# Performance work log

Measured on AMD Instinct MI355X. Metric: run time of the kernel, lower is better.

Reference implementation:

```python
import jax, jax.numpy as jnp
import numpy as np

CL = 64      # per-object feature dim
N = 8        # num objects/slots
B = 8192     # batch


def _init(key, fan_in, shape):
    # torch Linear default: U(-1/sqrt(fan_in), 1/sqrt(fan_in))
    bound = 1.0 / np.sqrt(fan_in)
    return jax.random.uniform(key, shape, jnp.float32, -bound, bound)


def setup_inputs() -> dict:
    key = jax.random.key(0)
    ks = jax.random.split(key, 20)
    inp = {
        "s": jax.random.normal(ks[0], (B, N, CL), jnp.float32),
        # weights stored (in, out); y = x @ W + b
        "W_enc": _init(ks[1], CL, (CL, CL)),   "b_enc": _init(ks[2], CL, (CL,)),
        "W_self0": _init(ks[3], CL, (CL, CL)), "b_self0": _init(ks[4], CL, (CL,)),
        "W_self1": _init(ks[5], CL, (CL, CL)), "b_self1": _init(ks[6], CL, (CL,)),
        "W_rel0": _init(ks[7], 2 * CL + 1, (2 * CL + 1, 2 * CL)), "b_rel0": _init(ks[8], 2 * CL + 1, (2 * CL,)),
        "W_rel1": _init(ks[9], 2 * CL, (2 * CL, CL)),             "b_rel1": _init(ks[10], 2 * CL, (CL,)),
        "W_rel2": _init(ks[11], CL, (CL, CL)),                    "b_rel2": _init(ks[12], CL, (CL,)),
        "W_att0": _init(ks[13], 2 * CL + 1, (2 * CL + 1, 2 * CL)), "b_att0": _init(ks[14], 2 * CL + 1, (2 * CL,)),
        "W_att1": _init(ks[15], 2 * CL, (2 * CL, CL)),             "b_att1": _init(ks[16], 2 * CL, (CL,)),
        "W_att2": _init(ks[17], CL, (CL, 1)),                      "b_att2": _init(ks[18], CL, (1,)),
    }
    return inp


def reference(s, W_enc, b_enc, W_self0, b_self0, W_self1, b_self1,
              W_rel0, b_rel0, W_rel1, b_rel1, W_rel2, b_rel2,
              W_att0, b_att0, W_att1, b_att1, W_att2, b_att2):
    elu = jax.nn.elu
    # keep first 2 coords (positions), re-encode the rest
    s = jnp.concatenate([s[..., :2], (s @ W_enc + b_enc)[..., 2:]], axis=-1)  # [B,N,CL]

    # self dynamics
    h = elu(s @ W_self0 + b_self0)
    self_dyn = h @ W_self1 + b_self1 + h                                      # [B,N,CL]

    # pairwise squared distances on first two coords: [B,N,N,1]
    pos = s[..., :2]
    dist = jnp.sum((pos[:, :, None, :] - pos[:, None, :, :]) ** 2, axis=-1, keepdims=True)

    # combinations = cat(arg1_i, arg2_j, dist). Split the first linear's weight rows
    # so we never materialize the [B,N,N,2CL+1] concat tensor.
    def pair_linear(W, b):
        Wa, Wb, Wd = W[:CL], W[CL:2 * CL], W[2 * CL]
        return (s @ Wa)[:, :, None, :] + (s @ Wb)[:, None, :, :] + dist * Wd + b

    rel_h1 = elu(pair_linear(W_rel0, b_rel0))        # [B,N,N,2CL]
    rel_h2 = elu(rel_h1 @ W_rel1 + b_rel1)           # [B,N,N,CL]
    rel_f = rel_h2 @ W_rel2 + b_rel2 + rel_h2        # [B,N,N,CL]

    att = elu(pair_linear(W_att0, b_att0))
    att = elu(att @ W_att1 + b_att1)
    att = jax.nn.sigmoid(att @ W_att2 + b_att2)      # [B,N,N,1]

    diag_mask = (1.0 - jnp.eye(N, dtype=s.dtype))[None, :, :, None]
    rel_dyn = jnp.sum(rel_f * diag_mask * att, axis=2)   # [B,N,CL]

    return jnp.sum(self_dyn + rel_dyn, axis=1)           # [B,CL]
```

## Files before the change

### kernel.cpp

```cpp
#include <hip/hip_runtime.h>
#include <math.h>

constexpr int NCL = 64;
constexpr int NN  = 8;
constexpr int NG  = 4;
constexpr int NT  = 1024;

typedef __attribute__((ext_vector_type(4))) float f32x4;
typedef __attribute__((ext_vector_type(8))) short s16x8;
#define MFMA __builtin_amdgcn_mfma_f32_16x16x32_bf16

constexpr int OFF_ENC = 0;
constexpr int OFF_S0  = 1024;
constexpr int OFF_S1  = 2048;
constexpr int OFF_R0  = 3072;
constexpr int OFF_A0  = 7168;
constexpr int OFF_A1  = 11264;
constexpr int OFF_R1  = 13312;

__device__ __forceinline__ float elu_f(float x) { return x > 0.f ? x : __expf(x) - 1.f; }

__device__ __forceinline__ short bfh_rn(float x) {
    union { float f; unsigned u; } c; c.f = x;
    return (short)((c.u + 0x7fffu + ((c.u >> 16) & 1u)) >> 16);
}
__device__ __forceinline__ void split_tr(float x, short& hi, short& lo) {
    union { float f; unsigned u; } c; c.f = x;
    hi = (short)(c.u >> 16);
    union { unsigned u; float f; } t; t.u = c.u & 0xffff0000u;
    lo = bfh_rn(x - t.f);
}

__device__ __forceinline__ void afrag_split(const float* act, int row, int kbase,
                                            s16x8& hi, s16x8& lo) {
    const float4 v0 = *(const float4*)(act + row * 68 + kbase);
    const float4 v1 = *(const float4*)(act + row * 68 + kbase + 4);
    float v[8] = {v0.x, v0.y, v0.z, v0.w, v1.x, v1.y, v1.z, v1.w};
    #pragma unroll
    for (int e = 0; e < 8; ++e) { short a, b; split_tr(v[e], a, b); hi[e] = a; lo[e] = b; }
}

__device__ __forceinline__ f32x4 node_tile_pk(const float* act, const s16x8* __restrict__ wb,
                                              int mt, int nt, int lane) {
    const int row = mt * 16 + (lane & 15);
    const int g   = lane >> 4;
    f32x4 acc = {0.f, 0.f, 0.f, 0.f};
    #pragma unroll
    for (int kg = 0; kg < 2; ++kg) {
        s16x8 ah, al;
        afrag_split(act, row, kg * 32 + g * 8, ah, al);
        const s16x8 bh = wb[(kg * 4 + nt) * 64 + lane];
        const s16x8 bl = wb[512 + (kg * 4 + nt) * 64 + lane];
        acc = MFMA(ah, bh, acc, 0, 0, 0);
        acc = MFMA(ah, bl, acc, 0, 0, 0);
        acc = MFMA(al, bh, acc, 0, 0, 0);
    }
    return acc;
}

__device__ __forceinline__ void x1frag(const float* Arow, const float* Brow,
                                       const float* wdg, float d, int fbase,
                                       s16x8& hi, s16x8& lo) {
    const float4 a0 = *(const float4*)(Arow + fbase);
    const float4 a1 = *(const float4*)(Arow + fbase + 4);
    const float4 c0 = *(const float4*)(Brow + fbase);
    const float4 c1 = *(const float4*)(Brow + fbase + 4);
    const float4 w0 = *(const float4*)(wdg + fbase);
    const float4 w1 = *(const float4*)(wdg + fbase + 4);
    float v[8];
    v[0] = elu_f(a0.x + c0.x + d * w0.x);
    v[1] = elu_f(a0.y + c0.y + d * w0.y);
    v[2] = elu_f(a0.z + c0.z + d * w0.z);
    v[3] = elu_f(a0.w + c0.w + d * w0.w);
    v[4] = elu_f(a1.x + c1.x + d * w1.x);
    v[5] = elu_f(a1.y + c1.y + d * w1.y);
    v[6] = elu_f(a1.z + c1.z + d * w1.z);
    v[7] = elu_f(a1.w + c1.w + d * w1.w);
    #pragma unroll
    for (int e = 0; e < 8; ++e) { short a, b; split_tr(v[e], a, b); hi[e] = a; lo[e] = b; }
}

__global__ __launch_bounds__(64)
void prep_kernel(const float* __restrict__ We,  const float* __restrict__ Ws0,
                 const float* __restrict__ Ws1, const float* __restrict__ Wr0,
                 const float* __restrict__ Wa0, const float* __restrict__ Wa1,
                 const float* __restrict__ Wr1, s16x8* __restrict__ ws)
{
    const int b = blockIdx.x, lane = threadIdx.x;
    const float* W; int nnt, nfrag, base, frag;
    if      (b < 8)   { W = We;  nnt = 4; nfrag = 8;  base = OFF_ENC; frag = b; }
    else if (b < 16)  { W = Ws0; nnt = 4; nfrag = 8;  base = OFF_S0;  frag = b - 8; }
    else if (b < 24)  { W = Ws1; nnt = 4; nfrag = 8;  base = OFF_S1;  frag = b - 16; }
    else if (b < 56)  { W = Wr0; nnt = 8; nfrag = 32; base = OFF_R0;  frag = b - 24; }
    else if (b < 88)  { W = Wa0; nnt = 8; nfrag = 32; base = OFF_A0;  frag = b - 56; }
    else if (b < 104) { W = Wa1; nnt = 4; nfrag = 16; base = OFF_A1;  frag = b - 88; }
    else              { W = Wr1; nnt = 4; nfrag = 16; base = OFF_R1;  frag = b - 104; }
    const int kg = frag / nnt, nt = frag % nnt;
    const int N  = nnt * 16;
    const int g  = lane >> 4, col = nt * 16 + (lane & 15);
    s16x8 hi, lo;
    #pragma unroll
    for (int e = 0; e < 8; ++e) {
        short a, c; split_tr(W[(kg * 32 + g * 8 + e) * N + col], a, c);
        hi[e] = a; lo[e] = c;
    }
    ws[base + frag * 64 + lane]              = hi;
    ws[base + nfrag * 64 + frag * 64 + lane] = lo;
}

__global__ __launch_bounds__(NT, 1)
void gh_kernel(const float* __restrict__ S,
               const float* __restrict__ b_enc,
               const float* __restrict__ b_self0, const float* __restrict__ b_self1,
               const float* __restrict__ W_rel0,  const float* __restrict__ b_rel0,
               const float* __restrict__ b_rel1,
               const float* __restrict__ W_rel2,  const float* __restrict__ b_rel2,
               const float* __restrict__ W_att0,  const float* __restrict__ b_att0,
               const float* __restrict__ b_att1,
               const float* __restrict__ W_att2,  const float* __restrict__ b_att2,
               const s16x8* __restrict__ wp,
               float* __restrict__ Out)
{
    __shared__ __align__(16) float sbuf[32 * 68];
    __shared__ __align__(16) float encb[32 * 68];
    __shared__ __align__(16) float hbuf[32 * 68];
    __shared__ __align__(16) float ABm[4][32 * 132];
    __shared__ __align__(16) s16x8 wstp[2048];
    __shared__ float d2l[4 * 64];
    __shared__ float cntl[32];
    __shared__ float Ubuf[4 * 68];
    __shared__ float wdl[2][128];

    const int tid  = threadIdx.x;
    const int w    = tid >> 6;
    const int lane = tid & 63;
    const int g    = lane >> 4;
    const int b0   = blockIdx.x * NG;
    float* sd = sbuf;
    float* Tb = hbuf;

    {
        const float* src = S + (size_t)b0 * NN * NCL;
        for (int idx = tid; idx < 32 * 64; idx += NT)
            sbuf[(idx >> 6) * 68 + (idx & 63)] = src[idx];
        for (int idx = tid; idx < 2048; idx += NT)
            wstp[idx] = wp[OFF_A1 + idx];
        if (tid < 128) {
            wdl[0][tid] = W_rel0[128 * 128 + tid];
            wdl[1][tid] = W_att0[128 * 128 + tid];
        }
    }
    __syncthreads();

    if (tid < 256) {
        const int bi = tid >> 6, i = (tid >> 3) & 7, j = tid & 7;
        const float dx = sbuf[(bi * 8 + i) * 68 + 0] - sbuf[(bi * 8 + j) * 68 + 0];
        const float dy = sbuf[(bi * 8 + i) * 68 + 1] - sbuf[(bi * 8 + j) * 68 + 1];
        d2l[bi * 64 + i * 8 + j] = dx * dx + dy * dy;
    }

    if (w < 8) {
        const int mt = w & 1, nt = w >> 1;
        f32x4 acc = node_tile_pk(sbuf, wp + OFF_ENC, mt, nt, lane);
        const int   col = nt * 16 + (lane & 15);
        const float be  = b_enc[col];
        #pragma unroll
        for (int reg = 0; reg < 4; ++reg) {
            const int row = mt * 16 + g * 4 + reg;
            float v = acc[reg] + be;
            if (col < 2) v = sbuf[row * 68 + col];
            encb[row * 68 + col] = v;
        }
    }
    __syncthreads();

    if (w < 8) {
        const int mt = w & 1, nt = w >> 1;
        f32x4 acc = node_tile_pk(encb, wp + OFF_S0, mt, nt, lane);
        const int   col = nt * 16 + (lane & 15);
        const float bs  = b_self0[col];
        #pragma unroll
        for (int reg = 0; reg < 4; ++reg)
            hbuf[(mt * 16 + g * 4 + reg) * 68 + col] = elu_f(acc[reg] + bs);
    }
    __syncthreads();

    if (w < 8) {
        const int mt = w & 1, nt = w >> 1;
        f32x4 acc = node_tile_pk(hbuf, wp + OFF_S1, mt, nt, lane);
        const int   col = nt * 16 + (lane & 15);
        const float bs  = b_self1[col];
        #pragma unroll
        for (int reg = 0; reg < 4; ++reg) {
            const int row = mt * 16 + g * 4 + reg;
            sd[row * 68 + col] = acc[reg] + bs + hbuf[row * 68 + col];
        }
    }
    {
        const int mtp = w >> 3, ntp = w & 7;
        const int row = mtp * 16 + (lane & 15);
        const int col = ntp * 16 + (lane & 15);
        s16x8 eh[2], el[2];
        afrag_split(encb, row, g * 8, eh[0], el[0]);
        afrag_split(encb, row, 32 + g * 8, eh[1], el[1]);
        #pragma unroll
        for (int m = 0; m < 4; ++m) {
            const s16x8* wb = wp + ((m < 2) ? OFF_R0 : OFF_A0);
            const int kgo = (m & 1) * 2;
            f32x4 acc = {0.f, 0.f, 0.f, 0.f};
            #pragma unroll
            for (int kg = 0; kg < 2; ++kg) {
                const s16x8 bh = wb[((kgo + kg) * 8 + ntp) * 64 + lane];
                const s16x8 bl = wb[2048 + ((kgo + kg) * 8 + ntp) * 64 + lane];
                acc = MFMA(eh[kg], bh, acc, 0, 0, 0);
                acc = MFMA(eh[kg], bl, acc, 0, 0, 0);
                acc = MFMA(el[kg], bh, acc, 0, 0, 0);
            }
            const float badd = (m == 0) ? b_rel0[col] : (m == 2) ? b_att0[col] : 0.f;
            #pragma unroll
            for (int reg = 0; reg < 4; ++reg)
                ABm[m][(mtp * 16 + g * 4 + reg) * 132 + col] = acc[reg] + badd;
        }
    }
    __syncthreads();

    const int bi    = w >> 2;
    const int ihalf = (w >> 1) & 1;
    const int mt    = w & 1;
    const int pp    = (lane & 15) + 16 * mt;
    const int il    = pp >> 3, jj8 = pp & 7;
    const float* Arow_a = &ABm[2][(bi * 8 + ihalf * 4 + il) * 132];
    const float* Brow_a = &ABm[3][(bi * 8 + jj8) * 132];
    const float* Arow_r = &ABm[0][(bi * 8 + ihalf * 4 + il) * 132];
    const float* Brow_r = &ABm[1][(bi * 8 + jj8) * 132];
    const float dpair   = d2l[bi * 64 + (ihalf * 4 + il) * 8 + jj8];

    float attreg[4];
    {
        const float ba2 = b_att2[0];
        float wa2v[4], ba1v[4];
        #pragma unroll
        for (int nt = 0; nt < 4; ++nt) {
            wa2v[nt] = W_att2[nt * 16 + (lane & 15)];
            ba1v[nt] = b_att1[nt * 16 + (lane & 15)];
        }
        s16x8 ah[4], al[4];
        #pragma unroll
        for (int kg = 0; kg < 4; ++kg)
            x1frag(Arow_a, Brow_a, &wdl[1][0], dpair, kg * 32 + g * 8, ah[kg], al[kg]);
        f32x4 acc[4];
        #pragma unroll
        for (int nt = 0; nt < 4; ++nt) {
            acc[nt] = {ba1v[nt], ba1v[nt], ba1v[nt], ba1v[nt]};
            #pragma unroll
            for (int kg = 0; kg < 4; ++kg) {
                const s16x8 bh = wstp[(kg * 4 + nt) * 64 + lane];
                const s16x8 bl = wstp[1024 + (kg * 4 + nt) * 64 + lane];
                acc[nt] = MFMA(ah[kg], bh, acc[nt], 0, 0, 0);
                acc[nt] = MFMA(ah[kg], bl, acc[nt], 0, 0, 0);
                acc[nt] = MFMA(al[kg], bh, acc[nt], 0, 0, 0);
            }
        }
        #pragma unroll
        for (int reg = 0; reg < 4; ++reg) {
            float s = 0.f;
            #pragma unroll
            for (int nt = 0; nt < 4; ++nt) s += elu_f(acc[nt][reg]) * wa2v[nt];
            s += __shfl_xor(s, 1, 64);
            s += __shfl_xor(s, 2, 64);
            s += __shfl_xor(s, 4, 64);
            s += __shfl_xor(s, 8, 64);
            attreg[reg] = 1.f / (1.f + __expf(-(s + ba2)));
        }
    }
    __syncthreads();

    for (int idx = tid; idx < 2048; idx += NT)
        wstp[idx] = wp[OFF_R1 + idx];
    __syncthreads();

    {
        float br1v[4];
        #pragma unroll
        for (int nt = 0; nt < 4; ++nt) br1v[nt] = b_rel1[nt * 16 + (lane & 15)];
        s16x8 ah[4], al[4];
        #pragma unroll
        for (int kg = 0; kg < 4; ++kg)
            x1frag(Arow_r, Brow_r, &wdl[0][0], dpair, kg * 32 + g * 8, ah[kg], al[kg]);
        f32x4 acc[4];
        #pragma unroll
        for (int nt = 0; nt < 4; ++nt) {
            acc[nt] = {br1v[nt], br1v[nt], br1v[nt], br1v[nt]};
            #pragma unroll
            for (int kg = 0; kg < 4; ++kg) {
                const s16x8 bh = wstp[(kg * 4 + nt) * 64 + lane];
                const s16x8 bl = wstp[1024 + (kg * 4 + nt) * 64 + lane];
                acc[nt] = MFMA(ah[kg], bh, acc[nt], 0, 0, 0);
                acc[nt] = MFMA(ah[kg], bl, acc[nt], 0, 0, 0);
                acc[nt] = MFMA(al[kg], bh, acc[nt], 0, 0, 0);
            }
        }
        const int ifull = ihalf * 4 + 2 * mt + (g >> 1);
        float coef[4], cpart = 0.f;
        #pragma unroll
        for (int reg = 0; reg < 4; ++reg) {
            const int jj = 4 * (g & 1) + reg;
            coef[reg] = (jj == ifull) ? 0.f : attreg[reg];
            cpart += coef[reg];
        }
        const float csum = cpart + __shfl_xor(cpart, 16, 64);
        if (((g & 1) == 0) && ((lane & 15) == 0))
            cntl[bi * 8 + ifull] = csum;
        #pragma unroll
        for (int nt = 0; nt < 4; ++nt) {
            float tpart = 0.f;
            #pragma unroll
            for (int reg = 0; reg < 4; ++reg)
                tpart += coef[reg] * elu_f(acc[nt][reg]);
            const float tsum = tpart + __shfl_xor(tpart, 16, 64);
            if ((g & 1) == 0)
                Tb[(bi * 8 + ifull) * 68 + nt * 16 + (lane & 15)] = tsum;
        }
    }
    __syncthreads();

    if (tid < 256) {
        const int b = tid >> 6, c = tid & 63;
        float u = 0.f;
        #pragma unroll
        for (int i = 0; i < 8; ++i) u += Tb[(b * 8 + i) * 68 + c];
        Ubuf[b * 68 + c] = u;
    }
    __syncthreads();

    if (tid < 256) {
        const int b = tid >> 6, c = tid & 63;
        float sds = 0.f, C = 0.f;
        #pragma unroll
        for (int i = 0; i < 8; ++i) {
            sds += sd[(b * 8 + i) * 68 + c];
            C   += cntl[b * 8 + i];
        }
        float r = 0.f;
        #pragma unroll 8
        for (int k = 0; k < 64; ++k)
            r += Ubuf[b * 68 + k] * W_rel2[k * 64 + c];
        Out[(size_t)(b0 + b) * 64 + c] = sds + r + C * b_rel2[c] + Ubuf[b * 68 + c];
    }
}

extern "C" void kernel_launch(void* const* d_in, const int* in_sizes, int n_in,
                              void* d_out, int out_size, void* d_ws, size_t ws_size,
                              hipStream_t stream) {
    const float* S       = (const float*)d_in[0];
    const float* W_enc   = (const float*)d_in[1];
    const float* b_enc   = (const float*)d_in[2];
    const float* W_self0 = (const float*)d_in[3];
    const float* b_self0 = (const float*)d_in[4];
    const float* W_self1 = (const float*)d_in[5];
    const float* b_self1 = (const float*)d_in[6];
    const float* W_rel0  = (const float*)d_in[7];
    const float* b_rel0  = (const float*)d_in[8];
    const float* W_rel1  = (const float*)d_in[9];
    const float* b_rel1  = (const float*)d_in[10];
    const float* W_rel2  = (const float*)d_in[11];
    const float* b_rel2  = (const float*)d_in[12];
    const float* W_att0  = (const float*)d_in[13];
    const float* b_att0  = (const float*)d_in[14];
    const float* W_att1  = (const float*)d_in[15];
    const float* b_att1  = (const float*)d_in[16];
    const float* W_att2  = (const float*)d_in[17];
    const float* b_att2  = (const float*)d_in[18];

    s16x8* wpk = (s16x8*)d_ws;

    prep_kernel<<<dim3(120), dim3(64), 0, stream>>>(
        W_enc, W_self0, W_self1, W_rel0, W_att0, W_att1, W_rel1, wpk);

    const int nB   = in_sizes[0] / (NN * NCL);
    const int grid = nB / NG;

    gh_kernel<<<dim3(grid), dim3(NT), 0, stream>>>(
        S, b_enc, b_self0, b_self1,
        W_rel0, b_rel0, b_rel1, W_rel2, b_rel2,
        W_att0, b_att0, b_att1, W_att2, b_att2,
        wpk, (float*)d_out);
}
```

Baseline: 245.0 us.

## Double-buffer pair weights in LDS, stream fragments, and use MFMA for rel2 projection

Keeps the att1 and rel1 packed weights in two separate LDS buffers so the mid-kernel reload and its two barriers go away. Builds the bf16 hi/lo activation fragments one k-group at a time using a perm-based pack, which lowers register pressure. The final W_rel2 projection moves from a scalar 64-term loop over global memory to split-bf16 MFMAs on weights packed by the prep kernel. This costs extra LDS and an additional barrier, and the lo-part rounding changes from round-to-nearest to truncation, with slight precision differences.

```diff
diff --git a/kernel.cpp b/kernel.cpp
--- a/kernel.cpp
+++ b/kernel.cpp
@@ -17,27 +17,31 @@
 constexpr int OFF_A0  = 7168;
 constexpr int OFF_A1  = 11264;
 constexpr int OFF_R1  = 13312;
+constexpr int OFF_R2  = 15360;
 
 __device__ __forceinline__ float elu_f(float x) { return x > 0.f ? x : __expf(x) - 1.f; }
 
-__device__ __forceinline__ short bfh_rn(float x) {
-    union { float f; unsigned u; } c; c.f = x;
-    return (short)((c.u + 0x7fffu + ((c.u >> 16) & 1u)) >> 16);
-}
-__device__ __forceinline__ void split_tr(float x, short& hi, short& lo) {
-    union { float f; unsigned u; } c; c.f = x;
-    hi = (short)(c.u >> 16);
-    union { unsigned u; float f; } t; t.u = c.u & 0xffff0000u;
-    lo = bfh_rn(x - t.f);
+__device__ __forceinline__ unsigned f2u(float x) { union { float f; unsigned u; } c; c.f = x; return c.u; }
+__device__ __forceinline__ float u2f(unsigned u) { union { unsigned u; float f; } c; c.u = u; return c.f; }
+
+__device__ __forceinline__ void splitpack8(const float v[8], s16x8& hi, s16x8& lo) {
+    union { s16x8 s; unsigned u[4]; } H, L;
+    #pragma unroll
+    for (int e = 0; e < 8; e += 2) {
+        H.u[e >> 1] = __builtin_amdgcn_perm(f2u(v[e + 1]), f2u(v[e]), 0x07060302u);
+        const float t0 = u2f(f2u(v[e])     & 0xffff0000u);
+        const float t1 = u2f(f2u(v[e + 1]) & 0xffff0000u);
+        L.u[e >> 1] = __builtin_amdgcn_perm(f2u(v[e + 1] - t1), f2u(v[e] - t0), 0x07060302u);
+    }
+    hi = H.s; lo = L.s;
 }
 
 __device__ __forceinline__ void afrag_split(const float* act, int row, int kbase,
                                             s16x8& hi, s16x8& lo) {
     const float4 v0 = *(const float4*)(act + row * 68 + kbase);
     const float4 v1 = *(const float4*)(act + row * 68 + kbase + 4);
-    float v[8] = {v0.x, v0.y, v0.z, v0.w, v1.x, v1.y, v1.z, v1.w};
-    #pragma unroll
-    for (int e = 0; e < 8; ++e) { short a, b; split_tr(v[e], a, b); hi[e] = a; lo[e] = b; }
+    const float v[8] = {v0.x, v0.y, v0.z, v0.w, v1.x, v1.y, v1.z, v1.w};
+    splitpack8(v, hi, lo);
 }
 
 __device__ __forceinline__ f32x4 node_tile_pk(const float* act, const s16x8* __restrict__ wb,
@@ -68,23 +72,34 @@
     const float4 w0 = *(const float4*)(wdg + fbase);
     const float4 w1 = *(const float4*)(wdg + fbase + 4);
     float v[8];
-    v[0] = elu_f(a0.x + c0.x + d * w0.x);
-    v[1] = elu_f(a0.y + c0.y + d * w0.y);
-    v[2] = elu_f(a0.z + c0.z + d * w0.z);
-    v[3] = elu_f(a0.w + c0.w + d * w0.w);
-    v[4] = elu_f(a1.x + c1.x + d * w1.x);
-    v[5] = elu_f(a1.y + c1.y + d * w1.y);
-    v[6] = elu_f(a1.z + c1.z + d * w1.z);
-    v[7] = elu_f(a1.w + c1.w + d * w1.w);
-    #pragma unroll
-    for (int e = 0; e < 8; ++e) { short a, b; split_tr(v[e], a, b); hi[e] = a; lo[e] = b; }
+    v[0] = elu_f(fmaf(d, w0.x, a0.x + c0.x));
+    v[1] = elu_f(fmaf(d, w0.y, a0.y + c0.y));
+    v[2] = elu_f(fmaf(d, w0.z, a0.z + c0.z));
+    v[3] = elu_f(fmaf(d, w0.w, a0.w + c0.w));
+    v[4] = elu_f(fmaf(d, w1.x, a1.x + c1.x));
+    v[5] = elu_f(fmaf(d, w1.y, a1.y + c1.y));
+    v[6] = elu_f(fmaf(d, w1.z, a1.z + c1.z));
+    v[7] = elu_f(fmaf(d, w1.w, a1.w + c1.w));
+    splitpack8(v, hi, lo);
+}
+
+__device__ __forceinline__ short bfh_rn(float x) {
+    union { float f; unsigned u; } c; c.f = x;
+    return (short)((c.u + 0x7fffu + ((c.u >> 16) & 1u)) >> 16);
+}
+__device__ __forceinline__ void split_tr(float x, short& hi, short& lo) {
+    union { float f; unsigned u; } c; c.f = x;
+    hi = (short)(c.u >> 16);
+    union { unsigned u; float f; } t; t.u = c.u & 0xffff0000u;
+    lo = bfh_rn(x - t.f);
 }
 
 __global__ __launch_bounds__(64)
 void prep_kernel(const float* __restrict__ We,  const float* __restrict__ Ws0,
                  const float* __restrict__ Ws1, const float* __restrict__ Wr0,
                  const float* __restrict__ Wa0, const float* __restrict__ Wa1,
-                 const float* __restrict__ Wr1, s16x8* __restrict__ ws)
+                 const float* __restrict__ Wr1, const float* __restrict__ Wr2,
+                 s16x8* __restrict__ ws)
 {
     const int b = blockIdx.x, lane = threadIdx.x;
     const float* W; int nnt, nfrag, base, frag;
@@ -94,7 +109,8 @@
     else if (b < 56)  { W = Wr0; nnt = 8; nfrag = 32; base = OFF_R0;  frag = b - 24; }
     else if (b < 88)  { W = Wa0; nnt = 8; nfrag = 32; base = OFF_A0;  frag = b - 56; }
     else if (b < 104) { W = Wa1; nnt = 4; nfrag = 16; base = OFF_A1;  frag = b - 88; }
-    else              { W = Wr1; nnt = 4; nfrag = 16; base = OFF_R1;  frag = b - 104; }
+    else if (b < 120) { W = Wr1; nnt = 4; nfrag = 16; base = OFF_R1;  frag = b - 104; }
+    else              { W = Wr2; nnt = 4; nfrag = 8;  base = OFF_R2;  frag = b - 120; }
     const int kg = frag / nnt, nt = frag % nnt;
     const int N  = nnt * 16;
     const int g  = lane >> 4, col = nt * 16 + (lane & 15);
@@ -113,8 +129,7 @@
                const float* __restrict__ b_enc,
                const float* __restrict__ b_self0, const float* __restrict__ b_self1,
                const float* __restrict__ W_rel0,  const float* __restrict__ b_rel0,
-               const float* __restrict__ b_rel1,
-               const float* __restrict__ W_rel2,  const float* __restrict__ b_rel2,
+               const float* __restrict__ b_rel1,  const float* __restrict__ b_rel2,
                const float* __restrict__ W_att0,  const float* __restrict__ b_att0,
                const float* __restrict__ b_att1,
                const float* __restrict__ W_att2,  const float* __restrict__ b_att2,
@@ -125,10 +140,10 @@
     __shared__ __align__(16) float encb[32 * 68];
     __shared__ __align__(16) float hbuf[32 * 68];
     __shared__ __align__(16) float ABm[4][32 * 132];
-    __shared__ __align__(16) s16x8 wstp[2048];
+    __shared__ __align__(16) s16x8 wstpA[2048];
+    __shared__ __align__(16) s16x8 wstpR[2048];
     __shared__ float d2l[4 * 64];
     __shared__ float cntl[32];
-    __shared__ float Ubuf[4 * 68];
     __shared__ float wdl[2][128];
 
     const int tid  = threadIdx.x;
@@ -136,15 +151,19 @@
     const int lane = tid & 63;
     const int g    = lane >> 4;
     const int b0   = blockIdx.x * NG;
-    float* sd = sbuf;
-    float* Tb = hbuf;
+    float* sd   = sbuf;
+    float* Tb   = hbuf;
+    float* Ubuf = encb;
+    float* Rbuf = encb + 512;
 
     {
         const float* src = S + (size_t)b0 * NN * NCL;
         for (int idx = tid; idx < 32 * 64; idx += NT)
             sbuf[(idx >> 6) * 68 + (idx & 63)] = src[idx];
-        for (int idx = tid; idx < 2048; idx += NT)
-            wstp[idx] = wp[OFF_A1 + idx];
+        for (int idx = tid; idx < 2048; idx += NT) {
+            wstpA[idx] = wp[OFF_A1 + idx];
+            wstpR[idx] = wp[OFF_R1 + idx];
+        }
         if (tid < 128) {
             wdl[0][tid] = W_rel0[128 * 128 + tid];
             wdl[1][tid] = W_att0[128 * 128 + tid];
@@ -238,27 +257,25 @@
     float attreg[4];
     {
         const float ba2 = b_att2[0];
-        float wa2v[4], ba1v[4];
+        float wa2v[4];
+        f32x4 acc[4];
         #pragma unroll
         for (int nt = 0; nt < 4; ++nt) {
             wa2v[nt] = W_att2[nt * 16 + (lane & 15)];
-            ba1v[nt] = b_att1[nt * 16 + (lane & 15)];
-        }
-        s16x8 ah[4], al[4];
-        #pragma unroll
-        for (int kg = 0; kg < 4; ++kg)
-            x1frag(Arow_a, Brow_a, &wdl[1][0], dpair, kg * 32 + g * 8, ah[kg], al[kg]);
-        f32x4 acc[4];
-        #pragma unroll
-        for (int nt = 0; nt < 4; ++nt) {
-            acc[nt] = {ba1v[nt], ba1v[nt], ba1v[nt], ba1v[nt]};
-            #pragma unroll
-            for (int kg = 0; kg < 4; ++kg) {
-                const s16x8 bh = wstp[(kg * 4 + nt) * 64 + lane];
-                const s16x8 bl = wstp[1024 + (kg * 4 + nt) * 64 + lane];
-                acc[nt] = MFMA(ah[kg], bh, acc[nt], 0, 0, 0);
-                acc[nt] = MFMA(ah[kg], bl, acc[nt], 0, 0, 0);
-                acc[nt] = MFMA(al[kg], bh, acc[nt], 0, 0, 0);
+            const float b1 = b_att1[nt * 16 + (lane & 15)];
+            acc[nt] = {b1, b1, b1, b1};
+        }
+        #pragma unroll
+        for (int kg = 0; kg < 4; ++kg) {
+            s16x8 ah, al;
+            x1frag(Arow_a, Brow_a, &wdl[1][0], dpair, kg * 32 + g * 8, ah, al);
+            #pragma unroll
+            for (int nt = 0; nt < 4; ++nt) {
+                const s16x8 bh = wstpA[(kg * 4 + nt) * 64 + lane];
+                const s16x8 bl = wstpA[1024 + (kg * 4 + nt) * 64 + lane];
+                acc[nt] = MFMA(ah, bh, acc[nt], 0, 0, 0);
+                acc[nt] = MFMA(ah, bl, acc[nt], 0, 0, 0);
+                acc[nt] = MFMA(al, bh, acc[nt], 0, 0, 0);
             }
         }
         #pragma unroll
@@ -273,31 +290,24 @@
             attreg[reg] = 1.f / (1.f + __expf(-(s + ba2)));
         }
     }
-    __syncthreads();
-
-    for (int idx = tid; idx < 2048; idx += NT)
-        wstp[idx] = wp[OFF_R1 + idx];
-    __syncthreads();
-
     {
-        float br1v[4];
-        #pragma unroll
-        for (int nt = 0; nt < 4; ++nt) br1v[nt] = b_rel1[nt * 16 + (lane & 15)];
-        s16x8 ah[4], al[4];
-        #pragma unroll
-        for (int kg = 0; kg < 4; ++kg)
-            x1frag(Arow_r, Brow_r, &wdl[0][0], dpair, kg * 32 + g * 8, ah[kg], al[kg]);
         f32x4 acc[4];
         #pragma unroll
         for (int nt = 0; nt < 4; ++nt) {
-            acc[nt] = {br1v[nt], br1v[nt], br1v[nt], br1v[nt]};
-            #pragma unroll
-            for (int kg = 0; kg < 4; ++kg) {
-                const s16x8 bh = wstp[(kg * 4 + nt) * 64 + lane];
-                const s16x8 bl = wstp[1024 + (kg * 4 + nt) * 64 + lane];
-                acc[nt] = MFMA(ah[kg], bh, acc[nt], 0, 0, 0);
-                acc[nt] = MFMA(ah[kg], bl, acc[nt], 0, 0, 0);
-                acc[nt] = MFMA(al[kg], bh, acc[nt], 0, 0, 0);
+            const float b1 = b_rel1[nt * 16 + (lane & 15)];
+            acc[nt] = {b1, b1, b1, b1};
+        }
+        #pragma unroll
+        for (int kg = 0; kg < 4; ++kg) {
+            s16x8 ah, al;
+            x1frag(Arow_r, Brow_r, &wdl[0][0], dpair, kg * 32 + g * 8, ah, al);
+            #pragma unroll
+            for (int nt = 0; nt < 4; ++nt) {
+                const s16x8 bh = wstpR[(kg * 4 + nt) * 64 + lane];
+                const s16x8 bl = wstpR[1024 + (kg * 4 + nt) * 64 + lane];
+                acc[nt] = MFMA(ah, bh, acc[nt], 0, 0, 0);
+                acc[nt] = MFMA(ah, bl, acc[nt], 0, 0, 0);
+                acc[nt] = MFMA(al, bh, acc[nt], 0, 0, 0);
             }
         }
         const int ifull = ihalf * 4 + 2 * mt + (g >> 1);
@@ -333,6 +343,34 @@
     }
     __syncthreads();
 
+    if (w < 4) {
+        const int nt2 = w;
+        f32x4 acc = {0.f, 0.f, 0.f, 0.f};
+        const int row = lane & 15;
+        #pragma unroll
+        for (int kg = 0; kg < 2; ++kg) {
+            float4 q0 = {0.f, 0.f, 0.f, 0.f}, q1 = {0.f, 0.f, 0.f, 0.f};
+            if (row < 4) {
+                q0 = *(const float4*)(Ubuf + row * 68 + kg * 32 + g * 8);
+                q1 = *(const float4*)(Ubuf + row * 68 + kg * 32 + g * 8 + 4);
+            }
+            const float v[8] = {q0.x, q0.y, q0.z, q0.w, q1.x, q1.y, q1.z, q1.w};
+            s16x8 uh, ul;
+            splitpack8(v, uh, ul);
+            const s16x8 bh = wp[OFF_R2 + (kg * 4 + nt2) * 64 + lane];
+            const s16x8 bl = wp[OFF_R2 + 512 + (kg * 4 + nt2) * 64 + lane];
+            acc = MFMA(uh, bh, acc, 0, 0, 0);
+            acc = MFMA(uh, bl, acc, 0, 0, 0);
+            acc = MFMA(ul, bh, acc, 0, 0, 0);
+        }
+        if (g == 0) {
+            #pragma unroll
+            for (int reg = 0; reg < 4; ++reg)
+                Rbuf[reg * 64 + nt2 * 16 + (lane & 15)] = acc[reg];
+        }
+    }
+    __syncthreads();
+
     if (tid < 256) {
         const int b = tid >> 6, c = tid & 63;
         float sds = 0.f, C = 0.f;
@@ -341,11 +379,7 @@
             sds += sd[(b * 8 + i) * 68 + c];
             C   += cntl[b * 8 + i];
         }
-        float r = 0.f;
-        #pragma unroll 8
-        for (int k = 0; k < 64; ++k)
-            r += Ubuf[b * 68 + k] * W_rel2[k * 64 + c];
-        Out[(size_t)(b0 + b) * 64 + c] = sds + r + C * b_rel2[c] + Ubuf[b * 68 + c];
+        Out[(size_t)(b0 + b) * 64 + c] = sds + Rbuf[b * 64 + c] + C * b_rel2[c] + Ubuf[b * 68 + c];
     }
 }
 
@@ -374,15 +408,15 @@
 
     s16x8* wpk = (s16x8*)d_ws;
 
-    prep_kernel<<<dim3(120), dim3(64), 0, stream>>>(
-        W_enc, W_self0, W_self1, W_rel0, W_att0, W_att1, W_rel1, wpk);
+    prep_kernel<<<dim3(128), dim3(64), 0, stream>>>(
+        W_enc, W_self0, W_self1, W_rel0, W_att0, W_att1, W_rel1, W_rel2, wpk);
 
     const int nB   = in_sizes[0] / (NN * NCL);
     const int grid = nB / NG;
 
     gh_kernel<<<dim3(grid), dim3(NT), 0, stream>>>(
         S, b_enc, b_self0, b_self1,
-        W_rel0, b_rel0, b_rel1, W_rel2, b_rel2,
+        W_rel0, b_rel0, b_rel1, b_rel2,
         W_att0, b_att0, b_att1, W_att2, b_att2,
         wpk, (float*)d_out);
 }
```

Result: faster. 223.6 us (-8.8%).
